# Kernel optimization log

Hardware: AMD Instinct MI355X
Metric: run time of the kernel (lower is better)

## Reference

```python
import jax, jax.numpy as jnp
import numpy as np

B, SQ, SK, D, H, DH = 4, 1024, 1024, 1024, 16, 64

def setup_inputs() -> dict:
    key = jax.random.key(0)
    ks = jax.random.split(key, 7)
    s = 0.02
    return {
        "input_ids": jax.random.normal(ks[0], (B, SQ, D), jnp.float32),
        "encoder_output": jax.random.normal(ks[1], (B, SK, D), jnp.float32),
        "position_bias": jax.random.normal(ks[2], (1, H, SQ, SK), jnp.float32),
        "Wq": jax.random.normal(ks[3], (D, H * DH), jnp.float32) * s,
        "Wk": jax.random.normal(ks[4], (D, H * DH), jnp.float32) * s,
        "Wv": jax.random.normal(ks[5], (D, H * DH), jnp.float32) * s,
        "Wo": jax.random.normal(ks[6], (H * DH, D), jnp.float32) * s,
    }

def reference(input_ids, encoder_output, position_bias, Wq, Wk, Wv, Wo):
    # bias-free projections (nn.Linear(..., bias=False))
    q = (input_ids @ Wq).reshape(B, SQ, H, DH).transpose(0, 2, 1, 3)      # [B,H,Sq,dh]
    k = (encoder_output @ Wk).reshape(B, SK, H, DH).transpose(0, 2, 1, 3)  # [B,H,Sk,dh]
    v = (encoder_output @ Wv).reshape(B, SK, H, DH).transpose(0, 2, 1, 3)  # [B,H,Sk,dh]
    # T5-style attention: NO 1/sqrt(dh) scaling, additive position bias
    scores = jnp.einsum("bhqd,bhkd->bhqk", q, k) + position_bias          # [B,H,Sq,Sk]
    attn = jax.nn.softmax(scores, axis=-1)
    ctx = jnp.einsum("bhqk,bhkd->bhqd", attn, v)                          # [B,H,Sq,dh]
    ctx = ctx.transpose(0, 2, 1, 3).reshape(B, SQ, H * DH)
    return ctx @ Wo                                                        # [B,Sq,D]
```

## Files before the change

### kernel.cpp

```cpp
#include <hip/hip_runtime.h>

typedef _Float16 f16;
typedef _Float16 f16x4 __attribute__((ext_vector_type(4)));
typedef _Float16 f16x8 __attribute__((ext_vector_type(8)));
typedef float f32x4 __attribute__((ext_vector_type(4)));

#define LOADLDS16(gp, lp)                                                     \
  __builtin_amdgcn_global_load_lds(                                           \
      (const __attribute__((address_space(1))) void*)(gp),                    \
      (__attribute__((address_space(3))) void*)(lp), 16, 0, 0)

__global__ __launch_bounds__(256) void k_cast2(const float* __restrict__ a,
                                               const float* __restrict__ b,
                                               f16* __restrict__ ya,
                                               f16* __restrict__ yb) {
  int i = blockIdx.x * 256 + threadIdx.x;
  const float* x;
  f16* y;
  if (i < 1048576) {
    x = a; y = ya;
  } else {
    x = b; y = yb; i -= 1048576;
  }
  float4 v = reinterpret_cast<const float4*>(x)[i];
  f16x4 o;
  o[0] = (f16)v.x; o[1] = (f16)v.y; o[2] = (f16)v.z; o[3] = (f16)v.w;
  reinterpret_cast<f16x4*>(y)[i] = o;
}

__global__ __launch_bounds__(256) void k_castw_t(
    const float* __restrict__ w0, const float* __restrict__ w1,
    const float* __restrict__ w2, const float* __restrict__ w3,
    f16* __restrict__ o0, f16* __restrict__ o1, f16* __restrict__ o2,
    f16* __restrict__ o3) {
  const float* W;
  f16* O;
  switch (blockIdx.z) {
    case 0: W = w0; O = o0; break;
    case 1: W = w1; O = o1; break;
    case 2: W = w2; O = o2; break;
    default: W = w3; O = o3; break;
  }
  __shared__ f16 T[64][72];
  const int tid = threadIdx.x;
  const int r0 = blockIdx.y * 64, c0 = blockIdx.x * 64;
#pragma unroll
  for (int i = 0; i < 4; ++i) {
    int c = i * 256 + tid;
    int row = c >> 4, col = (c & 15) * 4;
    float4 v = *reinterpret_cast<const float4*>(W + (size_t)(r0 + row) * 1024 + c0 + col);
    T[col + 0][row] = (f16)v.x;
    T[col + 1][row] = (f16)v.y;
    T[col + 2][row] = (f16)v.z;
    T[col + 3][row] = (f16)v.w;
  }
  __syncthreads();
#pragma unroll
  for (int i = 0; i < 2; ++i) {
    int c = i * 256 + tid;
    int cc = c >> 3, ro = (c & 7) * 8;
    f16x8 v;
#pragma unroll
    for (int j = 0; j < 8; ++j) v[j] = T[cc][ro + j];
    *reinterpret_cast<f16x8*>(O + (size_t)(c0 + cc) * 1024 + r0 + ro) = v;
  }
}

__global__ __launch_bounds__(256) void k_gemm_qkv(const f16* __restrict__ Xq,
                                                  const f16* __restrict__ Xkv,
                                                  const f16* __restrict__ Bt,
                                                  f16* __restrict__ outp) {
  __shared__ f16 As[128 * 64];
  __shared__ f16 Bs[128 * 64];
  const int tid = threadIdx.x;
  const int w = tid >> 6, l = tid & 63;
  const int lr = l & 15, lq = l >> 4;
  const int m0 = blockIdx.y * 128, n0 = blockIdx.x * 128;
  const f16* A = (n0 < 1024) ? Xq : Xkv;
  const int wr = (w >> 1) * 64, wc = (w & 1) * 64;
  const int K = 1024;
  f32x4 acc[4][4] = {};
  for (int kt = 0; kt < K; kt += 64) {
#pragma unroll
    for (int i = 0; i < 4; ++i) {
      int c = (i * 4 + w) * 64 + l;
      LOADLDS16(A + (size_t)(m0 + (c >> 3)) * K + kt + (c & 7) * 8,
                As + (size_t)(i * 4 + w) * 512);
      LOADLDS16(Bt + (size_t)(n0 + (c >> 3)) * K + kt + (c & 7) * 8,
                Bs + (size_t)(i * 4 + w) * 512);
    }
    __syncthreads();
#pragma unroll
    for (int kk = 0; kk < 2; ++kk) {
      f16x8 af[4], bf[4];
#pragma unroll
      for (int m = 0; m < 4; ++m)
        af[m] = *reinterpret_cast<const f16x8*>(As + (wr + m * 16 + lr) * 64 + kk * 32 + lq * 8);
#pragma unroll
      for (int n = 0; n < 4; ++n)
        bf[n] = *reinterpret_cast<const f16x8*>(Bs + (wc + n * 16 + lr) * 64 + kk * 32 + lq * 8);
#pragma unroll
      for (int m = 0; m < 4; ++m)
#pragma unroll
        for (int n = 0; n < 4; ++n)
          acc[m][n] = __builtin_amdgcn_mfma_f32_16x16x32_f16(af[m], bf[n], acc[m][n], 0, 0, 0);
    }
    __syncthreads();
  }
#pragma unroll
  for (int m = 0; m < 4; ++m)
#pragma unroll
    for (int n = 0; n < 4; ++n)
#pragma unroll
      for (int r = 0; r < 4; ++r) {
        int row = m0 + wr + m * 16 + lq * 4 + r;
        int col = n0 + wc + n * 16 + lr;
        int b = row >> 10, s = row & 1023;
        int plane = col >> 10, cc = col & 1023;
        int h = cc >> 6, dh = cc & 63;
        outp[(size_t)plane * 4194304 +
             (((size_t)(b * 16 + h)) * 1024 + s) * 64 + dh] = (f16)acc[m][n][r];
      }
}

__global__ __launch_bounds__(256) void k_gemm_o(const f16* __restrict__ A,
                                                const f16* __restrict__ Bt,
                                                float* __restrict__ out, int M,
                                                int N, int K) {
  __shared__ f16 As[64 * 64];
  __shared__ f16 Bs[128 * 64];
  const int tid = threadIdx.x;
  const int w = tid >> 6, l = tid & 63;
  const int lr = l & 15, lq = l >> 4;
  const int m0 = blockIdx.y * 64, n0 = blockIdx.x * 128;
  const int wr = (w >> 1) * 32, wc = (w & 1) * 64;
  f32x4 acc[2][4] = {};
  for (int kt = 0; kt < K; kt += 64) {
#pragma unroll
    for (int i = 0; i < 2; ++i) {
      int c = (i * 4 + w) * 64 + l;
      LOADLDS16(A + (size_t)(m0 + (c >> 3)) * K + kt + (c & 7) * 8,
                As + (size_t)(i * 4 + w) * 512);
    }
#pragma unroll
    for (int i = 0; i < 4; ++i) {
      int c = (i * 4 + w) * 64 + l;
      LOADLDS16(Bt + (size_t)(n0 + (c >> 3)) * K + kt + (c & 7) * 8,
                Bs + (size_t)(i * 4 + w) * 512);
    }
    __syncthreads();
#pragma unroll
    for (int kk = 0; kk < 2; ++kk) {
      f16x8 af[2], bf[4];
#pragma unroll
      for (int m = 0; m < 2; ++m)
        af[m] = *reinterpret_cast<const f16x8*>(As + (wr + m * 16 + lr) * 64 + kk * 32 + lq * 8);
#pragma unroll
      for (int n = 0; n < 4; ++n)
        bf[n] = *reinterpret_cast<const f16x8*>(Bs + (wc + n * 16 + lr) * 64 + kk * 32 + lq * 8);
#pragma unroll
      for (int m = 0; m < 2; ++m)
#pragma unroll
        for (int n = 0; n < 4; ++n)
          acc[m][n] = __builtin_amdgcn_mfma_f32_16x16x32_f16(af[m], bf[n], acc[m][n], 0, 0, 0);
    }
    __syncthreads();
  }
#pragma unroll
  for (int m = 0; m < 2; ++m)
#pragma unroll
    for (int n = 0; n < 4; ++n)
#pragma unroll
      for (int r = 0; r < 4; ++r) {
        int row = m0 + wr + m * 16 + lq * 4 + r;
        int col = n0 + wc + n * 16 + lr;
        out[(size_t)row * N + col] = acc[m][n][r];
      }
}

__global__ __launch_bounds__(256) void k_vtrans(const f16* __restrict__ vb,
                                                f16* __restrict__ vtb) {
  const int bh = blockIdx.y, s0 = blockIdx.x * 64;
  __shared__ f16 T[64][72];
  const int tid = threadIdx.x;
  const f16* src = vb + (size_t)bh * 1024 * 64;
#pragma unroll
  for (int i = 0; i < 2; ++i) {
    int c = i * 256 + tid;
    int row = c >> 3, co = (c & 7) * 8;
    f16x8 v = *reinterpret_cast<const f16x8*>(src + (size_t)(s0 + row) * 64 + co);
#pragma unroll
    for (int j = 0; j < 8; ++j) T[co + j][row] = v[j];
  }
  __syncthreads();
  f16* dst = vtb + (size_t)bh * 64 * 1024;
#pragma unroll
  for (int i = 0; i < 2; ++i) {
    int c = i * 256 + tid;
    int dh = c >> 3, so = (c & 7) * 8;
    f16x8 v;
#pragma unroll
    for (int j = 0; j < 8; ++j) v[j] = T[dh][so + j];
    *reinterpret_cast<f16x8*>(dst + (size_t)dh * 1024 + s0 + so) = v;
  }
}

__global__ __launch_bounds__(256) void k_attn(const f16* __restrict__ qb,
                                              const f16* __restrict__ kb,
                                              const f16* __restrict__ vtb,
                                              const float* __restrict__ bias,
                                              f16* __restrict__ ctx) {
  const int bid = blockIdx.x;
  const int ord = (bid & 7) * 128 + (bid >> 3);
  const int h = ord >> 6, qt = (ord >> 2) & 15, b = ord & 3;
  const int bh = b * 16 + h;
  const int q0 = qt * 64;
  const int tid = threadIdx.x, w = tid >> 6, l = tid & 63;
  const int lr = l & 15, lq = l >> 4;

  __shared__ f16 Kb[2][4096];
  __shared__ f16 Vb[2][4096];
  __shared__ f16 Ps[4][640];

  const f16* qp = qb + ((size_t)bh * 1024 + q0 + w * 16 + lr) * 64 + lq * 8;
  f16x8 qf0 = *reinterpret_cast<const f16x8*>(qp);
  f16x8 qf1 = *reinterpret_cast<const f16x8*>(qp + 32);

  f32x4 O[4] = {};
  float mrun = -3.0e38f, rsum = 0.f;

  const f16* kbase = kb + (size_t)bh * 65536;
  const f16* vbase = vtb + (size_t)bh * 65536;
  const float* bq = bias + ((size_t)h * 1024 + q0 + w * 16 + lr) * 1024 + lq * 4;

  auto stage = [&](int t, int nxt) {
#pragma unroll
    for (int i = 0; i < 2; ++i) {
      int c = (i * 4 + w) * 64 + l;
      int row = c >> 3, g = (c & 7) ^ (row & 7);
      LOADLDS16(kbase + (size_t)(t * 64 + row) * 64 + g * 8,
                &Kb[nxt][(i * 4 + w) * 512]);
      LOADLDS16(vbase + (size_t)row * 1024 + t * 64 + g * 8,
                &Vb[nxt][(i * 4 + w) * 512]);
    }
  };

  stage(0, 0);
  __syncthreads();

#pragma unroll 1
  for (int t = 0; t < 16; ++t) {
    const int cur = t & 1;
    if (t < 15) stage(t + 1, cur ^ 1);
    f32x4 bf[4];
#pragma unroll
    for (int c = 0; c < 4; ++c)
      bf[c] = *reinterpret_cast<const f32x4*>(bq + t * 64 + c * 16);
    __builtin_amdgcn_sched_barrier(0);

    f32x4 S[4] = {};
    __builtin_amdgcn_s_setprio(1);
#pragma unroll
    for (int c = 0; c < 4; ++c) {
      int row = c * 16 + lr;
      const f16* kbp = &Kb[cur][row * 64];
      f16x8 kf0 = *reinterpret_cast<const f16x8*>(kbp + ((lq ^ (row & 7)) * 8));
      f16x8 kf1 = *reinterpret_cast<const f16x8*>(kbp + (((4 + lq) ^ (row & 7)) * 8));
      S[c] = __builtin_amdgcn_mfma_f32_16x16x32_f16(kf0, qf0, S[c], 0, 0, 0);
      S[c] = __builtin_amdgcn_mfma_f32_16x16x32_f16(kf1, qf1, S[c], 0, 0, 0);
    }
    __builtin_amdgcn_s_setprio(0);

#pragma unroll
    for (int c = 0; c < 4; ++c)
#pragma unroll
      for (int r = 0; r < 4; ++r) S[c][r] += bf[c][r];

    float tmax = fmaxf(
        fmaxf(fmaxf(fmaxf(S[0][0], S[0][1]), fmaxf(S[0][2], S[0][3])),
              fmaxf(fmaxf(S[1][0], S[1][1]), fmaxf(S[1][2], S[1][3]))),
        fmaxf(fmaxf(fmaxf(S[2][0], S[2][1]), fmaxf(S[2][2], S[2][3])),
              fmaxf(fmaxf(S[3][0], S[3][1]), fmaxf(S[3][2], S[3][3]))));
    if (!__all(tmax <= mrun + 8.0f)) {
      tmax = fmaxf(tmax, __shfl_xor(tmax, 16, 64));
      tmax = fmaxf(tmax, __shfl_xor(tmax, 32, 64));
      float mnew = fmaxf(mrun, tmax);
      float sc = __expf(mrun - mnew);
      mrun = mnew;
      rsum *= sc;
      int sb = l & 48;
#pragma unroll
      for (int r = 0; r < 4; ++r) {
        float scO = __shfl(sc, sb | (lq * 4 + r), 64);
#pragma unroll
        for (int c = 0; c < 4; ++c) O[c][r] *= scO;
      }
    }

#pragma unroll
    for (int c = 0; c < 2; ++c) {
      f32x4 p;
#pragma unroll
      for (int r = 0; r < 4; ++r) p[r] = __expf(S[c][r] - mrun);
      rsum += (p[0] + p[1]) + (p[2] + p[3]);
      f16x4 ph = {(f16)p[0], (f16)p[1], (f16)p[2], (f16)p[3]};
      *reinterpret_cast<f16x4*>(&Ps[w][lr * 40 + c * 16 + lq * 4]) = ph;
    }
    f16x8 pa0 = *reinterpret_cast<const f16x8*>(&Ps[w][lr * 40 + lq * 8]);

#pragma unroll
    for (int c = 2; c < 4; ++c) {
      f32x4 p;
#pragma unroll
      for (int r = 0; r < 4; ++r) p[r] = __expf(S[c][r] - mrun);
      rsum += (p[0] + p[1]) + (p[2] + p[3]);
      f16x4 ph = {(f16)p[0], (f16)p[1], (f16)p[2], (f16)p[3]};
      *reinterpret_cast<f16x4*>(&Ps[w][lr * 40 + (c - 2) * 16 + lq * 4]) = ph;
    }
    f16x8 pa1 = *reinterpret_cast<const f16x8*>(&Ps[w][lr * 40 + lq * 8]);

    __builtin_amdgcn_s_setprio(1);
#pragma unroll
    for (int c = 0; c < 4; ++c) {
      int row = c * 16 + lr;
      const f16* vbp = &Vb[cur][row * 64];
      f16x8 vf0 = *reinterpret_cast<const f16x8*>(vbp + ((lq ^ (row & 7)) * 8));
      f16x8 vf1 = *reinterpret_cast<const f16x8*>(vbp + (((4 + lq) ^ (row & 7)) * 8));
      O[c] = __builtin_amdgcn_mfma_f32_16x16x32_f16(pa0, vf0, O[c], 0, 0, 0);
      O[c] = __builtin_amdgcn_mfma_f32_16x16x32_f16(pa1, vf1, O[c], 0, 0, 0);
    }
    __builtin_amdgcn_s_setprio(0);

    __syncthreads();
  }

  rsum += __shfl_xor(rsum, 16, 64);
  rsum += __shfl_xor(rsum, 32, 64);
  int sb = l & 48;
  float rs[4];
#pragma unroll
  for (int r = 0; r < 4; ++r) rs[r] = __shfl(rsum, sb | (lq * 4 + r), 64);

#pragma unroll
  for (int c = 0; c < 4; ++c)
#pragma unroll
    for (int r = 0; r < 4; ++r) {
      float o = O[c][r] / rs[r];
      int row = q0 + w * 16 + lq * 4 + r;
      ctx[((size_t)b * 1024 + row) * 1024 + h * 64 + c * 16 + lr] = (f16)o;
    }
}

extern "C" void kernel_launch(void* const* d_in, const int* in_sizes, int n_in,
                              void* d_out, int out_size, void* d_ws,
                              size_t ws_size, hipStream_t stream) {
  const float* input_ids = (const float*)d_in[0];
  const float* enc = (const float*)d_in[1];
  const float* bias = (const float*)d_in[2];
  const float* Wq = (const float*)d_in[3];
  const float* Wk = (const float*)d_in[4];
  const float* Wv = (const float*)d_in[5];
  const float* Wo = (const float*)d_in[6];

  char* ws = (char*)d_ws;
  const size_t MB = 1024 * 1024;
  f16* Xq  = (f16*)(ws + 0 * MB);
  f16* Xkv = (f16*)(ws + 8 * MB);
  f16* Wqt = (f16*)(ws + 16 * MB);
  f16* Wkt = (f16*)(ws + 18 * MB);
  f16* Wvt = (f16*)(ws + 20 * MB);
  f16* Wot = (f16*)(ws + 22 * MB);
  f16* qbuf = (f16*)(ws + 24 * MB);
  f16* kbuf = (f16*)(ws + 32 * MB);
  f16* vbuf = (f16*)(ws + 40 * MB);
  f16* vtb = Xkv;
  f16* ctxb = Xq;

  k_cast2<<<8192, 256, 0, stream>>>(input_ids, enc, Xq, Xkv);
  k_castw_t<<<dim3(16, 16, 4), 256, 0, stream>>>(Wq, Wk, Wv, Wo, Wqt, Wkt, Wvt, Wot);

  k_gemm_qkv<<<dim3(24, 32), 256, 0, stream>>>(Xq, Xkv, Wqt, qbuf);

  k_vtrans<<<dim3(16, 64), 256, 0, stream>>>(vbuf, vtb);

  k_attn<<<1024, 256, 0, stream>>>(qbuf, kbuf, vtb, bias, ctxb);

  k_gemm_o<<<dim3(8, 64), 256, 0, stream>>>(ctxb, Wot, (float*)d_out, 4096, 1024, 1024);
}
```

Before: 141.3 us.

## Write V transposed from QKV GEMM epilogue and keep P in registers

The QKV projection epilogue now writes the V plane directly in a [bh, dh, s] transposed layout with 4-wide f16 stores, so the separate V transpose kernel and its launch are removed. In the attention kernel, the softmax probabilities are packed into MFMA A-operand registers directly instead of going through an LDS round trip. To make the K index ordering match the register layout of P, the V fragments are now gathered as four 4-element LDS reads with a matching permutation. The risk is more, smaller LDS reads per step and scattered 8-byte global stores in the GEMM epilogue.

```diff
diff --git a/kernel.cpp b/kernel.cpp
--- a/kernel.cpp
+++ b/kernel.cpp
@@ -107,20 +107,31 @@
     }
     __syncthreads();
   }
+  const bool vplane = (n0 >= 2048);
 #pragma unroll
   for (int m = 0; m < 4; ++m)
 #pragma unroll
-    for (int n = 0; n < 4; ++n)
-#pragma unroll
-      for (int r = 0; r < 4; ++r) {
-        int row = m0 + wr + m * 16 + lq * 4 + r;
-        int col = n0 + wc + n * 16 + lr;
-        int b = row >> 10, s = row & 1023;
-        int plane = col >> 10, cc = col & 1023;
-        int h = cc >> 6, dh = cc & 63;
-        outp[(size_t)plane * 4194304 +
-             (((size_t)(b * 16 + h)) * 1024 + s) * 64 + dh] = (f16)acc[m][n][r];
+    for (int n = 0; n < 4; ++n) {
+      int col = n0 + wc + n * 16 + lr;
+      int row0 = m0 + wr + m * 16 + lq * 4;
+      int b = row0 >> 10, s0 = row0 & 1023;
+      int plane = col >> 10, cc = col & 1023;
+      int h = cc >> 6, dh = cc & 63;
+      if (vplane) {
+        f16x4 v4;
+#pragma unroll
+        for (int r = 0; r < 4; ++r) v4[r] = (f16)acc[m][n][r];
+        *reinterpret_cast<f16x4*>(
+            outp + (size_t)2 * 4194304 +
+            ((size_t)(b * 16 + h)) * 65536 + (size_t)dh * 1024 + s0) = v4;
+      } else {
+#pragma unroll
+        for (int r = 0; r < 4; ++r)
+          outp[(size_t)plane * 4194304 +
+               (((size_t)(b * 16 + h)) * 1024 + s0 + r) * 64 + dh] =
+              (f16)acc[m][n][r];
       }
+    }
 }
 
 __global__ __launch_bounds__(256) void k_gemm_o(const f16* __restrict__ A,
@@ -178,33 +189,6 @@
       }
 }
 
-__global__ __launch_bounds__(256) void k_vtrans(const f16* __restrict__ vb,
-                                                f16* __restrict__ vtb) {
-  const int bh = blockIdx.y, s0 = blockIdx.x * 64;
-  __shared__ f16 T[64][72];
-  const int tid = threadIdx.x;
-  const f16* src = vb + (size_t)bh * 1024 * 64;
-#pragma unroll
-  for (int i = 0; i < 2; ++i) {
-    int c = i * 256 + tid;
-    int row = c >> 3, co = (c & 7) * 8;
-    f16x8 v = *reinterpret_cast<const f16x8*>(src + (size_t)(s0 + row) * 64 + co);
-#pragma unroll
-    for (int j = 0; j < 8; ++j) T[co + j][row] = v[j];
-  }
-  __syncthreads();
-  f16* dst = vtb + (size_t)bh * 64 * 1024;
-#pragma unroll
-  for (int i = 0; i < 2; ++i) {
-    int c = i * 256 + tid;
-    int dh = c >> 3, so = (c & 7) * 8;
-    f16x8 v;
-#pragma unroll
-    for (int j = 0; j < 8; ++j) v[j] = T[dh][so + j];
-    *reinterpret_cast<f16x8*>(dst + (size_t)dh * 1024 + s0 + so) = v;
-  }
-}
-
 __global__ __launch_bounds__(256) void k_attn(const f16* __restrict__ qb,
                                               const f16* __restrict__ kb,
                                               const f16* __restrict__ vtb,
@@ -220,7 +204,6 @@
 
   __shared__ f16 Kb[2][4096];
   __shared__ f16 Vb[2][4096];
-  __shared__ f16 Ps[4][640];
 
   const f16* qp = qb + ((size_t)bh * 1024 + q0 + w * 16 + lr) * 64 + lq * 8;
   f16x8 qf0 = *reinterpret_cast<const f16x8*>(qp);
@@ -297,35 +280,40 @@
       }
     }
 
-#pragma unroll
-    for (int c = 0; c < 2; ++c) {
-      f32x4 p;
-#pragma unroll
-      for (int r = 0; r < 4; ++r) p[r] = __expf(S[c][r] - mrun);
-      rsum += (p[0] + p[1]) + (p[2] + p[3]);
-      f16x4 ph = {(f16)p[0], (f16)p[1], (f16)p[2], (f16)p[3]};
-      *reinterpret_cast<f16x4*>(&Ps[w][lr * 40 + c * 16 + lq * 4]) = ph;
-    }
-    f16x8 pa0 = *reinterpret_cast<const f16x8*>(&Ps[w][lr * 40 + lq * 8]);
-
-#pragma unroll
-    for (int c = 2; c < 4; ++c) {
-      f32x4 p;
-#pragma unroll
-      for (int r = 0; r < 4; ++r) p[r] = __expf(S[c][r] - mrun);
-      rsum += (p[0] + p[1]) + (p[2] + p[3]);
-      f16x4 ph = {(f16)p[0], (f16)p[1], (f16)p[2], (f16)p[3]};
-      *reinterpret_cast<f16x4*>(&Ps[w][lr * 40 + (c - 2) * 16 + lq * 4]) = ph;
-    }
-    f16x8 pa1 = *reinterpret_cast<const f16x8*>(&Ps[w][lr * 40 + lq * 8]);
+    f32x4 p[4];
+#pragma unroll
+    for (int c = 0; c < 4; ++c) {
+#pragma unroll
+      for (int r = 0; r < 4; ++r) p[c][r] = __expf(S[c][r] - mrun);
+      rsum += (p[c][0] + p[c][1]) + (p[c][2] + p[c][3]);
+    }
+    f16x8 pa0, pa1;
+#pragma unroll
+    for (int j = 0; j < 4; ++j) {
+      pa0[j] = (f16)p[0][j];
+      pa0[4 + j] = (f16)p[1][j];
+      pa1[j] = (f16)p[2][j];
+      pa1[4 + j] = (f16)p[3][j];
+    }
 
     __builtin_amdgcn_s_setprio(1);
 #pragma unroll
     for (int c = 0; c < 4; ++c) {
       int row = c * 16 + lr;
       const f16* vbp = &Vb[cur][row * 64];
-      f16x8 vf0 = *reinterpret_cast<const f16x8*>(vbp + ((lq ^ (row & 7)) * 8));
-      f16x8 vf1 = *reinterpret_cast<const f16x8*>(vbp + (((4 + lq) ^ (row & 7)) * 8));
+      int s8 = row & 7, sub = (lq & 1) * 4, gh = lq >> 1;
+      f16x4 v0 = *reinterpret_cast<const f16x4*>(vbp + ((gh ^ s8) * 8 + sub));
+      f16x4 v1 = *reinterpret_cast<const f16x4*>(vbp + (((2 + gh) ^ s8) * 8 + sub));
+      f16x4 v2 = *reinterpret_cast<const f16x4*>(vbp + (((4 + gh) ^ s8) * 8 + sub));
+      f16x4 v3 = *reinterpret_cast<const f16x4*>(vbp + (((6 + gh) ^ s8) * 8 + sub));
+      f16x8 vf0, vf1;
+#pragma unroll
+      for (int j = 0; j < 4; ++j) {
+        vf0[j] = v0[j];
+        vf0[4 + j] = v1[j];
+        vf1[j] = v2[j];
+        vf1[4 + j] = v3[j];
+      }
       O[c] = __builtin_amdgcn_mfma_f32_16x16x32_f16(pa0, vf0, O[c], 0, 0, 0);
       O[c] = __builtin_amdgcn_mfma_f32_16x16x32_f16(pa1, vf1, O[c], 0, 0, 0);
     }
@@ -372,8 +360,7 @@
   f16* Wot = (f16*)(ws + 22 * MB);
   f16* qbuf = (f16*)(ws + 24 * MB);
   f16* kbuf = (f16*)(ws + 32 * MB);
-  f16* vbuf = (f16*)(ws + 40 * MB);
-  f16* vtb = Xkv;
+  f16* vtb  = (f16*)(ws + 40 * MB);
   f16* ctxb = Xq;
 
   k_cast2<<<8192, 256, 0, stream>>>(input_ids, enc, Xq, Xkv);
@@ -381,8 +368,6 @@
 
   k_gemm_qkv<<<dim3(24, 32), 256, 0, stream>>>(Xq, Xkv, Wqt, qbuf);
 
-  k_vtrans<<<dim3(16, 64), 256, 0, stream>>>(vbuf, vtb);
-
   k_attn<<<1024, 256, 0, stream>>>(qbuf, kbuf, vtb, bias, ctxb);
 
   k_gemm_o<<<dim3(8, 64), 256, 0, stream>>>(ctxb, Wot, (float*)d_out, 4096, 1024, 1024);
```

After: 137.8 us. -2.5%, faster.
